# Kernel optimization log

Hardware: AMD Instinct MI355X
Metric: run time of the kernel (lower is better)

The kernel has to match this reference:

```python
import jax, jax.numpy as jnp
import numpy as np
import math

B, S, HID = 1, 4096, 2048
NH, NKV, DH = 8, 1, 256
ROPE_BASE = 10000.0


def setup_inputs() -> dict:
    key = jax.random.key(0)
    ks = jax.random.split(key, 5)
    sc = 0.02
    return {
        "hidden_states": jax.random.normal(ks[0], (B, S, HID), dtype=jnp.float32),
        "position_ids": jnp.arange(S, dtype=jnp.int32)[None, :].repeat(B, axis=0),
        "wq": jax.random.normal(ks[1], (HID, NH * DH), dtype=jnp.float32) * sc,
        "wk": jax.random.normal(ks[2], (HID, NKV * DH), dtype=jnp.float32) * sc,
        "wv": jax.random.normal(ks[3], (HID, NKV * DH), dtype=jnp.float32) * sc,
        "wo": jax.random.normal(ks[4], (NH * DH, HID), dtype=jnp.float32) * sc,
    }


def _rope_cos_sin(position_ids, dtype):
    # inv_freq: [DH/2]
    inv_freq = 1.0 / (ROPE_BASE ** (jnp.arange(0, DH, 2, dtype=jnp.float32) / DH))
    # freqs: [B, S, DH/2]
    freqs = position_ids.astype(jnp.float32)[:, :, None] * inv_freq[None, None, :]
    emb = jnp.concatenate([freqs, freqs], axis=-1)  # [B, S, DH]
    return jnp.cos(emb).astype(dtype), jnp.sin(emb).astype(dtype)


def _rotate_half(x):
    x1, x2 = x[..., : DH // 2], x[..., DH // 2 :]
    return jnp.concatenate([-x2, x1], axis=-1)


def reference(hidden_states, position_ids, wq, wk, wv, wo):
    bsz, q_len, _ = hidden_states.shape
    dtype = hidden_states.dtype

    # QKV projections (bias=False)
    q = (hidden_states @ wq).reshape(bsz, q_len, NH, DH).transpose(0, 2, 1, 3)   # [B,NH,S,DH]
    k = (hidden_states @ wk).reshape(bsz, q_len, NKV, DH).transpose(0, 2, 1, 3)  # [B,NKV,S,DH]
    v = (hidden_states @ wv).reshape(bsz, q_len, NKV, DH).transpose(0, 2, 1, 3)  # [B,NKV,S,DH]

    # RoPE (unsqueeze_dim=1 -> broadcast over heads)
    cos, sin = _rope_cos_sin(position_ids, dtype)
    cos, sin = cos[:, None, :, :], sin[:, None, :, :]  # [B,1,S,DH]
    q = q * cos + _rotate_half(q) * sin
    k = k * cos + _rotate_half(k) * sin

    # GQA: k/v broadcast over the NH head dim via matmul broadcasting (repeat_kv)
    scores = jnp.matmul(q, jnp.swapaxes(k, -1, -2)) / math.sqrt(DH)  # [B,NH,S,S]

    # additive causal mask (0 on/below diagonal, -inf-ish above)
    neg = jnp.finfo(jnp.float32).min
    causal = jnp.where(
        jnp.tril(jnp.ones((q_len, q_len), dtype=bool)), 0.0, neg
    ).astype(jnp.float32)[None, None, :, :]
    scores = scores + causal

    probs = jax.nn.softmax(scores.astype(jnp.float32), axis=-1).astype(dtype)
    attn = jnp.matmul(probs, v)  # [B,NH,S,DH] (v broadcasts over NH)

    attn = attn.transpose(0, 2, 1, 3).reshape(bsz, q_len, NH * DH)
    return attn @ wo
```

## Files before the change

### kernel.cpp

```cpp
#include <hip/hip_runtime.h>
#include <hip/hip_bf16.h>

typedef __bf16 bf16;
typedef __attribute__((ext_vector_type(8))) __bf16 bf16x8;
typedef __attribute__((ext_vector_type(4))) float f32x4;

#define S_LEN  4096
#define HIDDEN 2048
#define N_HEADS 8
#define D_HEAD 256
#define QKV_N  2560
#define NEG_BIG (-1e30f)
#define MFIX 8.0f

#define OFF_WQKVT 0u
#define OFF_WOT   10485760u
#define OFF_QKV   18874368u
#define OFF_VT    39845888u
#define OFF_AOUT  41943040u
#define OFF_FLAG  58720256u
#define WS_NEED   58720320u
#define OFF_PBUF  0u
#define OFF_LBUF  8388608u

__global__ __launch_bounds__(256) void detect_dtype(const unsigned short* __restrict__ w,
                                                    int* __restrict__ flag) {
  __shared__ int bad;
  if (threadIdx.x == 0) bad = 0;
  __syncthreads();
  int local = 0;
  for (int i = threadIdx.x; i < 4096; i += 256) {
    int e = (w[i] >> 7) & 0xFF;
    if (e >= 130) local = 1;
  }
  if (local) atomicOr(&bad, 1);
  __syncthreads();
  if (threadIdx.x == 0) *flag = bad;
}

__device__ __forceinline__ bf16x8 load8(const void* p, size_t idx, bool f32) {
  if (f32) {
    const float* q = (const float*)p + idx;
    bf16x8 r;
#pragma unroll
    for (int j = 0; j < 8; ++j) r[j] = (bf16)q[j];
    return r;
  }
  return *(const bf16x8*)((const bf16*)p + idx);
}

__device__ __forceinline__ void transpose_tile64(const void* __restrict__ src, size_t sbase,
                                                 int sld, bool f32,
                                                 bf16* __restrict__ dst, int dld,
                                                 bf16 (*T)[72]) {
  int tid = threadIdx.x;
  int r  = tid >> 2;
  int c4 = (tid & 3) * 16;
  *(bf16x8*)(&T[r][c4])     = load8(src, sbase + (size_t)r * sld + c4, f32);
  *(bf16x8*)(&T[r][c4 + 8]) = load8(src, sbase + (size_t)r * sld + c4 + 8, f32);
  __syncthreads();
  bf16x8 v0, v1;
#pragma unroll
  for (int j = 0; j < 8; ++j) { v0[j] = T[c4 + j][r]; v1[j] = T[c4 + 8 + j][r]; }
  *(bf16x8*)(dst + (size_t)r * dld + c4)     = v0;
  *(bf16x8*)(dst + (size_t)r * dld + c4 + 8) = v1;
}

__global__ __launch_bounds__(256) void build_wqkvT(const void* __restrict__ wq,
                                                   const void* __restrict__ wk,
                                                   const void* __restrict__ wv,
                                                   bf16* __restrict__ dst,
                                                   const int* __restrict__ flag) {
  __shared__ __align__(16) bf16 T[64][72];
  bool f32 = (*flag != 0);
  int n0 = blockIdx.x * 64;
  int k0 = blockIdx.y * 64;
  const void* src; int ld, c0;
  if (n0 < 2048)      { src = wq; ld = 2048; c0 = n0; }
  else if (n0 < 2304) { src = wk; ld = 256;  c0 = n0 - 2048; }
  else                { src = wv; ld = 256;  c0 = n0 - 2304; }
  transpose_tile64(src, (size_t)k0 * ld + c0, ld, f32,
                   dst + (size_t)n0 * HIDDEN + k0, HIDDEN, T);
}

__global__ __launch_bounds__(256) void transpose_any(const void* __restrict__ src, int sbase,
                                                     int sld,
                                                     bf16* __restrict__ dst, int dld,
                                                     const int* __restrict__ flag) {
  __shared__ __align__(16) bf16 T[64][72];
  bool f32 = flag && (*flag != 0);
  int c0 = blockIdx.x * 64;
  int r0 = blockIdx.y * 64;
  transpose_tile64(src, (size_t)sbase + (size_t)r0 * sld + c0, sld, f32,
                   dst + (size_t)c0 * dld + r0, dld, T);
}

__global__ __launch_bounds__(256) void gemm128(const void* __restrict__ A,
                                               const bf16* __restrict__ BT,
                                               void* __restrict__ C,
                                               int M, int N, int K,
                                               const int* __restrict__ aflag,
                                               const int* __restrict__ cflag) {
  __shared__ __align__(16) bf16 As[128][40];
  __shared__ __align__(16) bf16 Bs[128][40];
  bool af32 = aflag && (*aflag != 0);
  bool cf32 = cflag && (*cflag != 0);
  int tid  = threadIdx.x;
  int w = tid >> 6, lane = tid & 63;
  int quad = lane >> 4, l16 = lane & 15;
  int bm = blockIdx.y * 128, bn = blockIdx.x * 128;
  int wm = (w >> 1) * 64, wn = (w & 1) * 64;

  int sr = tid >> 2, sc = (tid & 3) * 8;
  size_t abase = (size_t)(bm + sr) * K + sc;
  const bf16* Bg = BT + (size_t)(bn + sr) * K + sc;

  f32x4 acc[4][4] = {};
  for (int kt = 0; kt < K; kt += 32) {
    bf16x8 a0 = load8(A, abase + kt, af32);
    bf16x8 a1 = load8(A, abase + kt + (size_t)64 * K, af32);
    bf16x8 b0 = *(const bf16x8*)(Bg + kt);
    bf16x8 b1 = *(const bf16x8*)(Bg + kt + (size_t)64 * K);
    __syncthreads();
    *(bf16x8*)(&As[sr][sc])      = a0;
    *(bf16x8*)(&As[sr + 64][sc]) = a1;
    *(bf16x8*)(&Bs[sr][sc])      = b0;
    *(bf16x8*)(&Bs[sr + 64][sc]) = b1;
    __syncthreads();
    bf16x8 af[4], bfr[4];
#pragma unroll
    for (int mt = 0; mt < 4; ++mt)
      af[mt] = *(const bf16x8*)(&As[wm + mt * 16 + l16][quad * 8]);
#pragma unroll
    for (int nt = 0; nt < 4; ++nt)
      bfr[nt] = *(const bf16x8*)(&Bs[wn + nt * 16 + l16][quad * 8]);
#pragma unroll
    for (int mt = 0; mt < 4; ++mt)
#pragma unroll
      for (int nt = 0; nt < 4; ++nt)
        acc[mt][nt] = __builtin_amdgcn_mfma_f32_16x16x32_bf16(af[mt], bfr[nt],
                                                              acc[mt][nt], 0, 0, 0);
  }
#pragma unroll
  for (int mt = 0; mt < 4; ++mt)
#pragma unroll
    for (int nt = 0; nt < 4; ++nt)
#pragma unroll
      for (int r = 0; r < 4; ++r) {
        int row = bm + wm + mt * 16 + quad * 4 + r;
        int col = bn + wn + nt * 16 + l16;
        size_t off = (size_t)row * N + col;
        float v = acc[mt][nt][r];
        if (cf32) ((float*)C)[off] = v;
        else      ((bf16*)C)[off] = (bf16)v;
      }
}

__global__ __launch_bounds__(256) void rope_kernel(bf16* __restrict__ qkv,
                                                   const int* __restrict__ pos) {
  int s = blockIdx.x;
  float p = (float)pos[s];
  bf16* row = qkv + (size_t)s * QKV_N;
  for (int i = threadIdx.x; i < 9 * 128; i += 256) {
    int h = i >> 7, d = i & 127;
    float inv = __expf(-(float)d * (9.210340371976184f / 128.0f));
    float th = p * inv;
    float sn, c;
    sincosf(th, &sn, &c);
    c  = (float)(bf16)c;
    sn = (float)(bf16)sn;
    bf16* x = row + ((h < 8) ? h * 256 : 2048);
    float x1 = (float)x[d], x2 = (float)x[d + 128];
    x[d]       = (bf16)(x1 * c - x2 * sn);
    x[d + 128] = (bf16)(x2 * c + x1 * sn);
  }
}

__global__ __launch_bounds__(256, 2) void attn_kernel(const bf16* __restrict__ qkv,
                                                      const bf16* __restrict__ VT,
                                                      bf16* __restrict__ aout,
                                                      bf16* __restrict__ pbuf,
                                                      float* __restrict__ lbuf) {
  __shared__ __align__(16) bf16 Ks[64 * 256];
  __shared__ __align__(16) bf16 Vs[256 * 64];
  __shared__ __align__(16) bf16 Pl[4][16][72];
  int tid  = threadIdx.x;
  int w = tid >> 6, lane = tid & 63;
  int quad = lane >> 4, l16 = lane & 15;
  int b    = blockIdx.x;
  int head = b & 7;
  int t    = b >> 3;
  int a    = t & 31, which = t >> 5;
  int qtBig = 63 - a;

  int nseg, sqt[2], sk0[2], sk1[2], smode[2];
  if (which == 0) {
    nseg = 1; sqt[0] = qtBig; sk0[0] = 0; sk1[0] = 33;
    smode[0] = (a == 31) ? 0 : 1;
  } else if (a == 31) {
    nseg = 1; sqt[0] = 31; sk0[0] = 0; sk1[0] = 32; smode[0] = 0;
  } else {
    nseg = 2;
    sqt[0] = qtBig; sk0[0] = 33; sk1[0] = qtBig + 1; smode[0] = 2;
    sqt[1] = a;     sk0[1] = 0;  sk1[1] = a + 1;     smode[1] = 0;
  }

  int kro = tid >> 5, kcc = tid & 31;
  int vro = tid >> 3, vcc = tid & 7;

  for (int sg = 0; sg < nseg; ++sg) {
    int qt = sqt[sg], k0 = sk0[sg], k1 = sk1[sg], mode = smode[sg];
    int qw = qt * 64 + w * 16;

    const bf16* qrow = qkv + (size_t)(qw + l16) * QKV_N + head * D_HEAD + quad * 8;
    bf16x8 qf[8];
#pragma unroll
    for (int dc = 0; dc < 8; ++dc) {
      bf16x8 tq = *(const bf16x8*)(qrow + dc * 32);
#pragma unroll
      for (int j = 0; j < 8; ++j) tq[j] = (bf16)((float)tq[j] * 0.0625f);
      qf[dc] = tq;
    }

    f32x4 o[16] = {};
    float lsum[4] = {0.f, 0.f, 0.f, 0.f};

    bf16x8 kpre[8], vpre[8];
    int kv0p = k0 << 6;
#pragma unroll
    for (int c = 0; c < 8; ++c) {
      kpre[c] = *(const bf16x8*)(qkv + (size_t)(kv0p + c * 8 + kro) * QKV_N + 2048 + kcc * 8);
      vpre[c] = *(const bf16x8*)(VT + (size_t)(c * 32 + vro) * S_LEN + kv0p + vcc * 8);
    }

    for (int kt = k0; kt < k1; ++kt) {
      __syncthreads();
#pragma unroll
      for (int c = 0; c < 8; ++c) {
        int r  = c * 8 + kro;
        *(bf16x8*)(Ks + r * 256 + ((kcc ^ (r & 31)) * 8)) = kpre[c];
        int rv = c * 32 + vro;
        *(bf16x8*)(Vs + rv * 64 + ((vcc ^ (rv & 7)) * 8)) = vpre[c];
      }
      __syncthreads();
      if (kt + 1 < k1) {
        int kv1 = (kt + 1) << 6;
#pragma unroll
        for (int c = 0; c < 8; ++c) {
          kpre[c] = *(const bf16x8*)(qkv + (size_t)(kv1 + c * 8 + kro) * QKV_N + 2048 + kcc * 8);
          vpre[c] = *(const bf16x8*)(VT + (size_t)(c * 32 + vro) * S_LEN + kv1 + vcc * 8);
        }
      }
      f32x4 sv[4] = {};
      __builtin_amdgcn_s_setprio(1);
#pragma unroll
      for (int dc = 0; dc < 8; ++dc)
#pragma unroll
        for (int n = 0; n < 4; ++n) {
          int row = n * 16 + l16;
          bf16x8 kf = *(const bf16x8*)(Ks + row * 256 + (((dc << 2) + quad) ^ (row & 31)) * 8);
          sv[n] = __builtin_amdgcn_mfma_f32_16x16x32_bf16(qf[dc], kf, sv[n], 0, 0, 0);
        }
      __builtin_amdgcn_s_setprio(0);
      bool diag = (kt == qt);
      float pv4[4][4];
#pragma unroll
      for (int n = 0; n < 4; ++n)
#pragma unroll
        for (int r = 0; r < 4; ++r) {
          float x = sv[n][r] - MFIX;
          if (diag && (n * 16 + l16 > w * 16 + quad * 4 + r)) x = NEG_BIG;
          float e = __expf(x);
          pv4[n][r] = e;
          lsum[r] += e;
        }
#pragma unroll
      for (int n = 0; n < 4; ++n)
#pragma unroll
        for (int r = 0; r < 4; ++r)
          Pl[w][quad * 4 + r][n * 16 + l16] = (bf16)pv4[n][r];
      asm volatile("s_waitcnt lgkmcnt(0)" ::: "memory");
      bf16x8 pa0 = *(const bf16x8*)(&Pl[w][l16][quad * 8]);
      bf16x8 pa1 = *(const bf16x8*)(&Pl[w][l16][32 + quad * 8]);
      __builtin_amdgcn_s_setprio(1);
#pragma unroll
      for (int dt = 0; dt < 16; ++dt) {
        int row = dt * 16 + l16;
        const bf16* vb = Vs + row * 64;
        bf16x8 v0 = *(const bf16x8*)(vb + ((quad)     ^ (row & 7)) * 8);
        bf16x8 v1 = *(const bf16x8*)(vb + ((4 + quad) ^ (row & 7)) * 8);
        o[dt] = __builtin_amdgcn_mfma_f32_16x16x32_bf16(pa0, v0, o[dt], 0, 0, 0);
        o[dt] = __builtin_amdgcn_mfma_f32_16x16x32_bf16(pa1, v1, o[dt], 0, 0, 0);
      }
      __builtin_amdgcn_s_setprio(0);
    }

    float lrow[4];
#pragma unroll
    for (int r = 0; r < 4; ++r) lrow[r] = lsum[r];
#pragma unroll
    for (int off = 8; off >= 1; off >>= 1)
#pragma unroll
      for (int r = 0; r < 4; ++r)
        lrow[r] += __shfl_xor(lrow[r], off, 16);

    if (mode == 0) {
      float invl[4];
#pragma unroll
      for (int r = 0; r < 4; ++r) invl[r] = 1.0f / lrow[r];
      bf16* orow = aout + (size_t)(qw + quad * 4) * HIDDEN + head * D_HEAD + l16;
#pragma unroll
      for (int dt = 0; dt < 16; ++dt)
#pragma unroll
        for (int r = 0; r < 4; ++r)
          orow[(size_t)r * HIDDEN + dt * 16] = (bf16)(o[dt][r] * invl[r]);
    } else {
      if (mode == 1) {
        bf16* orow = aout + (size_t)(qw + quad * 4) * HIDDEN + head * D_HEAD + l16;
#pragma unroll
        for (int dt = 0; dt < 16; ++dt)
#pragma unroll
          for (int r = 0; r < 4; ++r)
            orow[(size_t)r * HIDDEN + dt * 16] = (bf16)o[dt][r];
      } else {
        int pidx = head * 31 + a;
        bf16* orow = pbuf + ((size_t)pidx * 64 + w * 16 + quad * 4) * 256 + l16;
#pragma unroll
        for (int dt = 0; dt < 16; ++dt)
#pragma unroll
          for (int r = 0; r < 4; ++r)
            orow[(size_t)r * 256 + dt * 16] = (bf16)o[dt][r];
      }
      if (l16 == 0) {
        int pidx = head * 31 + a;
        int base = (pidx * 2 + which) * 64 + w * 16 + quad * 4;
#pragma unroll
        for (int r = 0; r < 4; ++r) lbuf[base + r] = lrow[r];
      }
    }
  }
}

__global__ __launch_bounds__(256) void combine_kernel(bf16* __restrict__ aout,
                                                      const bf16* __restrict__ pbuf,
                                                      const float* __restrict__ lbuf) {
  int p = blockIdx.x;
  int h = p / 31, a = p % 31;
  int qtBig = 63 - a;
  int tid = threadIdx.x;
  for (int i = tid; i < 2048; i += 256) {
    int rowin = i >> 5;
    int d8 = (i & 31) * 8;
    int row = qtBig * 64 + rowin;
    float l = lbuf[(p * 2 + 0) * 64 + rowin] + lbuf[(p * 2 + 1) * 64 + rowin];
    float inv = 1.0f / l;
    bf16* ap = aout + (size_t)row * HIDDEN + h * D_HEAD + d8;
    const bf16* bp = pbuf + ((size_t)p * 64 + rowin) * 256 + d8;
    bf16x8 va = *(const bf16x8*)ap;
    bf16x8 vb = *(const bf16x8*)bp;
    bf16x8 vo;
#pragma unroll
    for (int j = 0; j < 8; ++j)
      vo[j] = (bf16)(((float)va[j] + (float)vb[j]) * inv);
    *(bf16x8*)ap = vo;
  }
}

extern "C" void kernel_launch(void* const* d_in, const int* in_sizes, int n_in,
                              void* d_out, int out_size, void* d_ws, size_t ws_size,
                              hipStream_t stream) {
  if (ws_size < (size_t)WS_NEED) return;
  const void* hs  = d_in[0];
  const int*  pos = (const int*)d_in[1];
  const void* wq  = d_in[2];
  const void* wk  = d_in[3];
  const void* wv  = d_in[4];
  const void* wo  = d_in[5];

  char* ws = (char*)d_ws;
  bf16* wqkvT = (bf16*)(ws + OFF_WQKVT);
  bf16* woT   = (bf16*)(ws + OFF_WOT);
  bf16* qkv   = (bf16*)(ws + OFF_QKV);
  bf16* VT    = (bf16*)(ws + OFF_VT);
  bf16* aout  = (bf16*)(ws + OFF_AOUT);
  int*  flag  = (int*)(ws + OFF_FLAG);
  bf16*  pbuf = (bf16*)(ws + OFF_PBUF);
  float* lbuf = (float*)(ws + OFF_LBUF);

  detect_dtype<<<1, 256, 0, stream>>>((const unsigned short*)wq, flag);
  build_wqkvT<<<dim3(QKV_N / 64, HIDDEN / 64), 256, 0, stream>>>(wq, wk, wv, wqkvT, flag);
  transpose_any<<<dim3(HIDDEN / 64, HIDDEN / 64), 256, 0, stream>>>(wo, 0, HIDDEN,
                                                                    woT, HIDDEN, flag);
  gemm128<<<dim3(QKV_N / 128, S_LEN / 128), 256, 0, stream>>>(hs, wqkvT, qkv,
                                                              S_LEN, QKV_N, HIDDEN,
                                                              flag, nullptr);
  rope_kernel<<<S_LEN, 256, 0, stream>>>(qkv, pos);
  transpose_any<<<dim3(D_HEAD / 64, S_LEN / 64), 256, 0, stream>>>(qkv, 2304, QKV_N,
                                                                   VT, S_LEN, nullptr);
  attn_kernel<<<N_HEADS * 64, 256, 0, stream>>>(qkv, VT, aout, pbuf, lbuf);
  combine_kernel<<<248, 256, 0, stream>>>(aout, pbuf, lbuf);
  gemm128<<<dim3(HIDDEN / 128, S_LEN / 128), 256, 0, stream>>>(aout, woT, d_out,
                                                               S_LEN, HIDDEN, HIDDEN,
                                                               nullptr, flag);
}
```

Baseline: 408.5 us.

## Rewrite GEMM with direct-to-LDS async loads, double buffering and BK=64

Replaces the register-staged 128x128x32 GEMM with a 128x128x64 kernel that uses global_load_lds to copy tiles straight into XOR-swizzled, double-buffered LDS. The next K tile is prefetched while MFMAs run on the current one, and only one barrier is needed per iteration. Because the direct LDS path needs bf16 input, a separate cvt_hs kernel first converts hidden_states into the aout scratch buffer. This adds an extra pass over memory and doubles LDS use per block, which may reduce occupancy.

```diff
diff --git a/kernel.cpp b/kernel.cpp
--- a/kernel.cpp
+++ b/kernel.cpp
@@ -47,6 +47,14 @@
     return r;
   }
   return *(const bf16x8*)((const bf16*)p + idx);
+}
+
+__global__ __launch_bounds__(256) void cvt_hs(const void* __restrict__ hs,
+                                              bf16* __restrict__ dst,
+                                              const int* __restrict__ flag) {
+  bool f32 = (*flag != 0);
+  size_t i = ((size_t)blockIdx.x * 256 + threadIdx.x) * 8;
+  *(bf16x8*)(dst + i) = load8(hs, i, f32);
 }
 
 __device__ __forceinline__ void transpose_tile64(const void* __restrict__ src, size_t sbase,
@@ -95,15 +103,19 @@
                    dst + (size_t)c0 * dld + r0, dld, T);
 }
 
-__global__ __launch_bounds__(256) void gemm128(const void* __restrict__ A,
-                                               const bf16* __restrict__ BT,
-                                               void* __restrict__ C,
-                                               int M, int N, int K,
-                                               const int* __restrict__ aflag,
-                                               const int* __restrict__ cflag) {
-  __shared__ __align__(16) bf16 As[128][40];
-  __shared__ __align__(16) bf16 Bs[128][40];
-  bool af32 = aflag && (*aflag != 0);
+__device__ __forceinline__ void gload16(const bf16* g, bf16* l) {
+  __builtin_amdgcn_global_load_lds((__attribute__((address_space(1))) void*)(void*)g,
+                                   (__attribute__((address_space(3))) void*)(void*)l,
+                                   16, 0, 0);
+}
+
+__global__ __launch_bounds__(256) void gemm_bk64(const bf16* __restrict__ A,
+                                                 const bf16* __restrict__ BT,
+                                                 void* __restrict__ C,
+                                                 int M, int N, int K,
+                                                 const int* __restrict__ cflag) {
+  __shared__ __align__(16) bf16 As[2][128 * 64];
+  __shared__ __align__(16) bf16 Bs[2][128 * 64];
   bool cf32 = cflag && (*cflag != 0);
   int tid  = threadIdx.x;
   int w = tid >> 6, lane = tid & 63;
@@ -111,36 +123,61 @@
   int bm = blockIdx.y * 128, bn = blockIdx.x * 128;
   int wm = (w >> 1) * 64, wn = (w & 1) * 64;
 
-  int sr = tid >> 2, sc = (tid & 3) * 8;
-  size_t abase = (size_t)(bm + sr) * K + sc;
-  const bf16* Bg = BT + (size_t)(bn + sr) * K + sc;
+  int lr = lane >> 3, lc = lane & 7;
+  int scol = ((lc ^ lr) << 3);
+  const bf16* Ag[4]; const bf16* Bg[4];
+#pragma unroll
+  for (int j = 0; j < 4; ++j) {
+    int row = (w * 4 + j) * 8 + lr;
+    Ag[j] = A  + (size_t)(bm + row) * K + scol;
+    Bg[j] = BT + (size_t)(bn + row) * K + scol;
+  }
+
+  int nIter = K >> 6;
+#pragma unroll
+  for (int j = 0; j < 4; ++j) {
+    gload16(Ag[j], &As[0][(w * 4 + j) * 512]);
+    gload16(Bg[j], &Bs[0][(w * 4 + j) * 512]);
+  }
+  __syncthreads();
+
+  int cA = ((quad    ) ^ (l16 & 7)) << 3;
+  int cB = ((quad + 4) ^ (l16 & 7)) << 3;
 
   f32x4 acc[4][4] = {};
-  for (int kt = 0; kt < K; kt += 32) {
-    bf16x8 a0 = load8(A, abase + kt, af32);
-    bf16x8 a1 = load8(A, abase + kt + (size_t)64 * K, af32);
-    bf16x8 b0 = *(const bf16x8*)(Bg + kt);
-    bf16x8 b1 = *(const bf16x8*)(Bg + kt + (size_t)64 * K);
+  for (int kt = 0; kt < nIter; ++kt) {
+    int cur = kt & 1;
+    if (kt + 1 < nIter) {
+      int nxt = cur ^ 1;
+      int koff = (kt + 1) << 6;
+#pragma unroll
+      for (int j = 0; j < 4; ++j) {
+        gload16(Ag[j] + koff, &As[nxt][(w * 4 + j) * 512]);
+        gload16(Bg[j] + koff, &Bs[nxt][(w * 4 + j) * 512]);
+      }
+    }
+    const bf16* Ab = &As[cur][0];
+    const bf16* Bb = &Bs[cur][0];
+#pragma unroll
+    for (int h = 0; h < 2; ++h) {
+      int cc = h ? cB : cA;
+      bf16x8 af[4], bfr[4];
+#pragma unroll
+      for (int mt = 0; mt < 4; ++mt)
+        af[mt] = *(const bf16x8*)(Ab + (wm + mt * 16 + l16) * 64 + cc);
+#pragma unroll
+      for (int nt = 0; nt < 4; ++nt)
+        bfr[nt] = *(const bf16x8*)(Bb + (wn + nt * 16 + l16) * 64 + cc);
+#pragma unroll
+      for (int mt = 0; mt < 4; ++mt)
+#pragma unroll
+        for (int nt = 0; nt < 4; ++nt)
+          acc[mt][nt] = __builtin_amdgcn_mfma_f32_16x16x32_bf16(af[mt], bfr[nt],
+                                                                acc[mt][nt], 0, 0, 0);
+    }
     __syncthreads();
-    *(bf16x8*)(&As[sr][sc])      = a0;
-    *(bf16x8*)(&As[sr + 64][sc]) = a1;
-    *(bf16x8*)(&Bs[sr][sc])      = b0;
-    *(bf16x8*)(&Bs[sr + 64][sc]) = b1;
-    __syncthreads();
-    bf16x8 af[4], bfr[4];
-#pragma unroll
-    for (int mt = 0; mt < 4; ++mt)
-      af[mt] = *(const bf16x8*)(&As[wm + mt * 16 + l16][quad * 8]);
-#pragma unroll
-    for (int nt = 0; nt < 4; ++nt)
-      bfr[nt] = *(const bf16x8*)(&Bs[wn + nt * 16 + l16][quad * 8]);
-#pragma unroll
-    for (int mt = 0; mt < 4; ++mt)
-#pragma unroll
-      for (int nt = 0; nt < 4; ++nt)
-        acc[mt][nt] = __builtin_amdgcn_mfma_f32_16x16x32_bf16(af[mt], bfr[nt],
-                                                              acc[mt][nt], 0, 0, 0);
-  }
+  }
+
 #pragma unroll
   for (int mt = 0; mt < 4; ++mt)
 #pragma unroll
@@ -386,20 +423,22 @@
   int*  flag  = (int*)(ws + OFF_FLAG);
   bf16*  pbuf = (bf16*)(ws + OFF_PBUF);
   float* lbuf = (float*)(ws + OFF_LBUF);
+  bf16*  hsb  = aout;
 
   detect_dtype<<<1, 256, 0, stream>>>((const unsigned short*)wq, flag);
   build_wqkvT<<<dim3(QKV_N / 64, HIDDEN / 64), 256, 0, stream>>>(wq, wk, wv, wqkvT, flag);
   transpose_any<<<dim3(HIDDEN / 64, HIDDEN / 64), 256, 0, stream>>>(wo, 0, HIDDEN,
                                                                     woT, HIDDEN, flag);
-  gemm128<<<dim3(QKV_N / 128, S_LEN / 128), 256, 0, stream>>>(hs, wqkvT, qkv,
-                                                              S_LEN, QKV_N, HIDDEN,
-                                                              flag, nullptr);
+  cvt_hs<<<(S_LEN * HIDDEN) / (256 * 8), 256, 0, stream>>>(hs, hsb, flag);
+  gemm_bk64<<<dim3(QKV_N / 128, S_LEN / 128), 256, 0, stream>>>(hsb, wqkvT, qkv,
+                                                                S_LEN, QKV_N, HIDDEN,
+                                                                nullptr);
   rope_kernel<<<S_LEN, 256, 0, stream>>>(qkv, pos);
   transpose_any<<<dim3(D_HEAD / 64, S_LEN / 64), 256, 0, stream>>>(qkv, 2304, QKV_N,
                                                                    VT, S_LEN, nullptr);
   attn_kernel<<<N_HEADS * 64, 256, 0, stream>>>(qkv, VT, aout, pbuf, lbuf);
   combine_kernel<<<248, 256, 0, stream>>>(aout, pbuf, lbuf);
-  gemm128<<<dim3(HIDDEN / 128, S_LEN / 128), 256, 0, stream>>>(aout, woT, d_out,
-                                                               S_LEN, HIDDEN, HIDDEN,
-                                                               nullptr, flag);
-}
+  gemm_bk64<<<dim3(HIDDEN / 128, S_LEN / 128), 256, 0, stream>>>(aout, woT, d_out,
+                                                                 S_LEN, HIDDEN, HIDDEN,
+                                                                 flag);
+}
```

Result: faster. 355.4 us (-13.0%).
